# Kernel tuning notes

Measured on AMD Instinct MI355X. Metric: run time of the kernel, lower is better.

The kernel has to match this reference:

```python
import jax, jax.numpy as jnp
import numpy as np

IMG_W = 224
STRIDE = 16
NUM_HEADS = 12
# 196 grid centers, x-major order: [(x, y) for x in ... for y in ...]
_xs = np.arange(STRIDE // 2, IMG_W, STRIDE)
GRIDS = jnp.asarray(np.array([(x, y) for x in _xs for y in _xs], dtype=np.float32))  # [196, 2]


def setup_inputs() -> dict:
    key = jax.random.key(0)
    ks = jax.random.split(key, 8)
    B, N, C = 256, 198, 768
    s = 0.02
    return {
        "x": jax.random.normal(ks[0], (B, N, C), dtype=jnp.float32),
        "w_qkv": jax.random.normal(ks[1], (C, 3 * C), dtype=jnp.float32) * s,  # qkv_bias=False
        "w_proj": jax.random.normal(ks[2], (C, C), dtype=jnp.float32) * s,
        "b_proj": jax.random.normal(ks[3], (C,), dtype=jnp.float32) * s,
        "w_D": jax.random.normal(ks[4], (C, 3), dtype=jnp.float32) * s,
        "b_D": jax.random.normal(ks[5], (3,), dtype=jnp.float32) * s,
        "w_cen": jax.random.normal(ks[6], (C, 6), dtype=jnp.float32) * s,
        "b_cen": jax.random.normal(ks[7], (6,), dtype=jnp.float32) * s,
    }


def reference(x, w_qkv, w_proj, b_proj, w_D, b_D, w_cen, b_cen):
    B, N, C = x.shape
    H = NUM_HEADS
    dh = C // H
    scale = dh ** (-0.5)

    qkv = (x @ w_qkv).reshape(B, N, 3, H, dh).transpose(2, 0, 3, 1, 4)  # [3,B,H,N,dh]
    q, k, v = qkv[0], qkv[1], qkv[2]

    attn = jnp.einsum('bhnd,bhmd->bhnm', q, k) * scale
    attn = jax.nn.softmax(attn, axis=-1)  # [B,H,N,N]

    # CLS-token query, heads concatenated: q.permute(2,0,1,3).reshape(N,B,C)[0]
    q0 = q[:, :, 0, :].reshape(B, C)
    D = IMG_W * jax.nn.sigmoid(q0 @ w_D + b_D)                      # [B,3]
    cen = jax.nn.sigmoid((q0 @ w_cen + b_cen).reshape(B, 3, 2))     # [B,3,2]

    # mixture-of-gaussian blobs over 196 patch grid positions
    sigma = (D / 2.0)[..., None]                                    # [B,3,1]
    coord = cen * (IMG_W - 1)                                       # [B,3,2]
    dist = ((coord[:, :, None, :] - GRIDS[None, None]) ** 2).sum(-1)  # [B,3,196]
    mgb = jnp.exp(-dist / (2.0 * sigma ** 2)) / 2.0 / 3.14 / sigma ** 2
    mgb = mgb / mgb.sum(-1, keepdims=True)
    mgb = mgb.sum(axis=1) / 3.0                                     # [B,196]
    mgb = jnp.concatenate([jnp.ones((B, 2), mgb.dtype), mgb], axis=1)  # [B,N]

    # head-score reweighting of the CLS attention row
    hs = attn[:, :, 0, :].transpose(1, 0, 2)   # [H,B,N] == permute(1,2,0,3) squeezed
    hs = hs * mgb[None]                        # broadcast over heads
    hs = hs / hs.sum(-1, keepdims=True)
    # replicate torch masked_scatter flat-order semantics:
    # source flattened in (h,b,n) order is written into target positions in (b,h,n) order
    new_row = hs.reshape(-1).reshape(B, H, N)
    attn = attn.at[:, :, 0, :].set(new_row)

    out = jnp.einsum('bhnm,bhmd->bhnd', attn, v)      # [B,H,N,dh]
    out = out.transpose(0, 2, 1, 3).reshape(B, N, C)
    out = out @ w_proj + b_proj
    return cen, attn[:, :, 0, :], out
```

## Files before the change

### kernel.cpp

```cpp
#include <hip/hip_runtime.h>
#include <cstdint>
#include <cstddef>

typedef __attribute__((ext_vector_type(4))) float  f32x4;
typedef __attribute__((ext_vector_type(8))) __bf16 bf16x8;
typedef __attribute__((ext_vector_type(4))) __bf16 bf16x4;

#define MFMA16(A, B, C) __builtin_amdgcn_mfma_f32_16x16x32_bf16((A), (B), (C), 0, 0, 0)

#define GLOAD_LDS16(gp, lp)                                        \
    __builtin_amdgcn_global_load_lds(                              \
        (const __attribute__((address_space(1))) void*)(gp),       \
        (__attribute__((address_space(3))) void*)(lp), 16, 0, 0)

#define NB 256
#define NN 198
#define NC 768
#define NH 12

__global__ __launch_bounds__(256) void cast_to_bf16(const float* __restrict__ in,
                                                    __bf16* __restrict__ out, int n8) {
    int i = blockIdx.x * 256 + threadIdx.x;
    if (i < n8) {
        const float4 f0 = reinterpret_cast<const float4*>(in)[i * 2];
        const float4 f1 = reinterpret_cast<const float4*>(in)[i * 2 + 1];
        bf16x8 h;
        h[0] = (__bf16)f0.x; h[1] = (__bf16)f0.y; h[2] = (__bf16)f0.z; h[3] = (__bf16)f0.w;
        h[4] = (__bf16)f1.x; h[5] = (__bf16)f1.y; h[6] = (__bf16)f1.z; h[7] = (__bf16)f1.w;
        reinterpret_cast<bf16x8*>(out)[i] = h;
    }
}

__global__ __launch_bounds__(256) void transpose_to_bf16(
    const float* __restrict__ in, __bf16* __restrict__ out, int R, int Cc) {
    __shared__ __bf16 tile[32][33];
    const int ntc = Cc >> 5;
    const int tc = blockIdx.x % ntc, tr = blockIdx.x / ntc;
    const int c0 = tc * 32, r0 = tr * 32;
    const int lx = threadIdx.x & 31, ly = threadIdx.x >> 5;
#pragma unroll
    for (int j = 0; j < 4; ++j)
        tile[ly + j * 8][lx] = (__bf16)in[(size_t)(r0 + ly + j * 8) * Cc + c0 + lx];
    __syncthreads();
#pragma unroll
    for (int j = 0; j < 4; ++j)
        out[(size_t)(c0 + ly + j * 8) * R + r0 + lx] = tile[lx][ly + j * 8];
}

__global__ __launch_bounds__(512, 2) void gemm_qkv_v7(
    const __bf16* __restrict__ xb, const __bf16* __restrict__ wT,
    __bf16* __restrict__ qb, __bf16* __restrict__ kb, __bf16* __restrict__ vb,
    float* __restrict__ q0) {
    __shared__ __bf16 As[2][256 * 64];
    __shared__ __bf16 Bs[2][256 * 64];
    const int bid = blockIdx.x;
    const int xcd = bid & 7, lin = bid >> 3;
    const int wgid = (xcd < 6 ? xcd * 223 : 6 * 223 + (xcd - 6) * 222) + lin;
    const int brow = (wgid / 9) * 256;
    const int bcol = (wgid % 9) * 256;
    const int tid = threadIdx.x, lane = tid & 63, wid = tid >> 6;
    const int wr = wid >> 2, wc = wid & 3;
    const int lr = lane & 15, lg = lane >> 4;

    const int srow = tid >> 3;
    const int sslot = (tid & 7) ^ ((tid >> 3) & 7);
    const __bf16* aSrc = xb + (size_t)(brow + srow) * 768 + sslot * 8;
    const __bf16* bSrc = wT + (size_t)(bcol + srow) * 768 + sslot * 8;
    const int key = lr & 7;

    f32x4 acc[8][4] = {};

#define STAGE7(buf, kk0)                                                       \
    {                                                                          \
        __bf16* aD = &As[buf][wid * 512];                                      \
        __bf16* bD = &Bs[buf][wid * 512];                                      \
        _Pragma("unroll")                                                      \
        for (int j = 0; j < 4; ++j) {                                          \
            GLOAD_LDS16(aSrc + (size_t)j * 64 * 768 + (kk0), aD + j * 4096);   \
            GLOAD_LDS16(bSrc + (size_t)j * 64 * 768 + (kk0), bD + j * 4096);   \
        }                                                                      \
    }

#define LDA7(f0, f1, f2, f3, m0)                                               \
    f0 = *reinterpret_cast<const bf16x8*>(                                     \
        Ab + (wr * 128 + (m0) * 16 + lr) * 64 + ((lg ^ key) * 8));             \
    f1 = *reinterpret_cast<const bf16x8*>(                                     \
        Ab + (wr * 128 + (m0) * 16 + lr) * 64 + (((4 + lg) ^ key) * 8));       \
    f2 = *reinterpret_cast<const bf16x8*>(                                     \
        Ab + (wr * 128 + (m0) * 16 + 16 + lr) * 64 + ((lg ^ key) * 8));        \
    f3 = *reinterpret_cast<const bf16x8*>(                                     \
        Ab + (wr * 128 + (m0) * 16 + 16 + lr) * 64 + (((4 + lg) ^ key) * 8));

#define MFMA_PHASE7(f0, f1, f2, f3, m0)                                        \
    __builtin_amdgcn_s_setprio(1);                                             \
    _Pragma("unroll")                                                          \
    for (int nt = 0; nt < 4; ++nt) acc[(m0)][nt]     = MFMA16(f0, bfr[0][nt], acc[(m0)][nt]);     \
    _Pragma("unroll")                                                          \
    for (int nt = 0; nt < 4; ++nt) acc[(m0)][nt]     = MFMA16(f1, bfr[1][nt], acc[(m0)][nt]);     \
    _Pragma("unroll")                                                          \
    for (int nt = 0; nt < 4; ++nt) acc[(m0) + 1][nt] = MFMA16(f2, bfr[0][nt], acc[(m0) + 1][nt]); \
    _Pragma("unroll")                                                          \
    for (int nt = 0; nt < 4; ++nt) acc[(m0) + 1][nt] = MFMA16(f3, bfr[1][nt], acc[(m0) + 1][nt]); \
    __builtin_amdgcn_s_setprio(0);

    STAGE7(0, 0);
    STAGE7(1, 64);
    for (int tau = 0; tau < 12; ++tau) {
        const int b = tau & 1;
        if (tau == 11) asm volatile("s_waitcnt vmcnt(0)" ::: "memory");
        else           asm volatile("s_waitcnt vmcnt(8)" ::: "memory");
        __builtin_amdgcn_s_barrier();
        __builtin_amdgcn_sched_barrier(0);
        const __bf16* Ab = As[b];
        const __bf16* Bb = Bs[b];
        bf16x8 bfr[2][4];
#pragma unroll
        for (int kk = 0; kk < 2; ++kk)
#pragma unroll
            for (int nt = 0; nt < 4; ++nt)
                bfr[kk][nt] = *reinterpret_cast<const bf16x8*>(
                    Bb + (wc * 64 + nt * 16 + lr) * 64 + (((kk * 4 + lg) ^ key) * 8));
        bf16x8 a0, a1, a2, a3, b0, b1, b2, b3;
        LDA7(a0, a1, a2, a3, 0);
        LDA7(b0, b1, b2, b3, 2);
        asm volatile("s_waitcnt lgkmcnt(4)" ::: "memory");
        __builtin_amdgcn_sched_barrier(0);
        MFMA_PHASE7(a0, a1, a2, a3, 0);
        LDA7(a0, a1, a2, a3, 4);
        asm volatile("s_waitcnt lgkmcnt(4)" ::: "memory");
        __builtin_amdgcn_sched_barrier(0);
        MFMA_PHASE7(b0, b1, b2, b3, 2);
        LDA7(b0, b1, b2, b3, 6);
        asm volatile("s_waitcnt lgkmcnt(4)" ::: "memory");
        __builtin_amdgcn_sched_barrier(0);
        MFMA_PHASE7(a0, a1, a2, a3, 4);
        asm volatile("s_waitcnt lgkmcnt(0)" ::: "memory");
        __builtin_amdgcn_sched_barrier(0);
        __builtin_amdgcn_s_barrier();
        __builtin_amdgcn_sched_barrier(0);
        if (tau < 10) STAGE7(b, (tau + 2) * 64);
        MFMA_PHASE7(b0, b1, b2, b3, 6);
    }
#undef STAGE7

#pragma unroll
    for (int mt = 0; mt < 8; ++mt) {
        int grow0 = brow + wr * 128 + mt * 16 + lg * 4;
        int bbs[4], nns[4];
#pragma unroll
        for (int r = 0; r < 4; ++r) {
            bbs[r] = (grow0 + r) / 198;
            nns[r] = (grow0 + r) % 198;
        }
#pragma unroll
        for (int nt = 0; nt < 4; ++nt) {
            int gcol = bcol + wc * 64 + nt * 16 + lr;
            int sidx = gcol / 768;
            int rem  = gcol % 768;
            __bf16* dstbuf = (sidx == 0) ? qb : (sidx == 1) ? kb : vb;
            int hh = rem >> 6, dd = rem & 63;
#pragma unroll
            for (int r = 0; r < 4; ++r) {
                float val = acc[mt][nt][r];
                dstbuf[(((size_t)bbs[r] * 12 + hh) * 198 + nns[r]) * 64 + dd] = (__bf16)val;
                if (sidx == 0 && nns[r] == 0) q0[bbs[r] * 768 + rem] = val;
            }
        }
    }
}

__global__ __launch_bounds__(256) void mgb_kernel(
    const float* __restrict__ q0, const float* __restrict__ wD,
    const float* __restrict__ bD, const float* __restrict__ wcen,
    const float* __restrict__ bcen, float* __restrict__ cen_out,
    float* __restrict__ mgb) {
    const int b = blockIdx.x, t = threadIdx.x;
    __shared__ float qs[768];
    __shared__ float red[256];
    __shared__ float vals[9];
    qs[t]       = q0[b * 768 + t];
    qs[t + 256] = q0[b * 768 + t + 256];
    qs[t + 512] = q0[b * 768 + t + 512];
    __syncthreads();
    for (int j = 0; j < 9; ++j) {
        float p;
        if (j < 3)
            p = qs[t] * wD[t * 3 + j] + qs[t + 256] * wD[(t + 256) * 3 + j] +
                qs[t + 512] * wD[(t + 512) * 3 + j];
        else {
            int c = j - 3;
            p = qs[t] * wcen[t * 6 + c] + qs[t + 256] * wcen[(t + 256) * 6 + c] +
                qs[t + 512] * wcen[(t + 512) * 6 + c];
        }
        red[t] = p;
        __syncthreads();
        for (int off = 128; off > 0; off >>= 1) {
            if (t < off) red[t] += red[t + off];
            __syncthreads();
        }
        if (t == 0) {
            float bias = (j < 3) ? bD[j] : bcen[j - 3];
            vals[j] = 1.f / (1.f + __expf(-(red[0] + bias)));
        }
        __syncthreads();
    }
    if (t < 6) cen_out[b * 6 + t] = vals[3 + t];

    float e3[3] = {0.f, 0.f, 0.f};
    if (t < 196) {
        float gx = 8.f + 16.f * (float)(t / 14);
        float gy = 8.f + 16.f * (float)(t % 14);
#pragma unroll
        for (int j = 0; j < 3; ++j) {
            float sig = 112.f * vals[j];
            float cx = vals[3 + 2 * j] * 223.f;
            float cy = vals[3 + 2 * j + 1] * 223.f;
            float dx = cx - gx, dy = cy - gy;
            e3[j] = __expf(-(dx * dx + dy * dy) / (2.f * sig * sig));
        }
    }
    float js[3];
    for (int j = 0; j < 3; ++j) {
        red[t] = e3[j];
        __syncthreads();
        for (int off = 128; off > 0; off >>= 1) {
            if (t < off) red[t] += red[t + off];
            __syncthreads();
        }
        js[j] = red[0];
        __syncthreads();
    }
    if (t < 196) {
        float m = (e3[0] / js[0] + e3[1] / js[1] + e3[2] / js[2]) * (1.f / 3.f);
        mgb[(size_t)b * 198 + 2 + t] = m;
    }
    if (t < 2) mgb[(size_t)b * 198 + t] = 1.f;
}

__global__ __launch_bounds__(256) void attn_kernel(
    const __bf16* __restrict__ qb, const __bf16* __restrict__ kb,
    const __bf16* __restrict__ vb, float* __restrict__ p0,
    __bf16* __restrict__ outp) {
    __shared__ __bf16 Klds[208 * 64];
    __shared__ __bf16 Vt[64][216];
    __shared__ __bf16 Plds[4][16][216];
    const int bh = blockIdx.x;
    const int b = bh / 12, h = bh % 12;
    const __bf16* Qp = qb + (size_t)bh * NN * 64;
    const __bf16* Kp = kb + (size_t)bh * NN * 64;
    const __bf16* Vp = vb + (size_t)bh * NN * 64;
    const int tid = threadIdx.x, lane = tid & 63, wid = tid >> 6;
    const int lr = lane & 15, lg = lane >> 4;

    {
        const int rsub = wid * 8 + (lane >> 3);
        const int sl   = ((lane & 7) ^ ((lane >> 3) & 7)) * 8;
#pragma unroll
        for (int i = 0; i < 7; ++i) {
            if (i < 6 || wid < 2) {
                int row = i * 32 + rsub;
                int rowc = row < 198 ? row : 197;
                GLOAD_LDS16(Kp + (size_t)rowc * 64 + sl,
                            Klds + (size_t)i * 2048 + wid * 512);
            }
        }
    }

    for (int i = tid; i < 104 * 8; i += 256) {
        int key2 = (i >> 3) * 2, d0 = (i & 7) << 3;
        int kr0 = key2 < 198 ? key2 : 197;
        int kr1 = key2 + 1 < 198 ? key2 + 1 : 197;
        bf16x8 h0 = *reinterpret_cast<const bf16x8*>(Vp + kr0 * 64 + d0);
        bf16x8 h1 = *reinterpret_cast<const bf16x8*>(Vp + kr1 * 64 + d0);
#pragma unroll
        for (int j = 0; j < 8; ++j) {
            union { __bf16 hh[2]; unsigned u; } pk;
            pk.hh[0] = h0[j]; pk.hh[1] = h1[j];
            *reinterpret_cast<unsigned*>(&Vt[d0 + j][key2]) = pk.u;
        }
    }
    __syncthreads();

    for (int ch = wid; ch < 13; ch += 4) {
        int n0 = ch * 16;
        int qrow = n0 + lr; if (qrow > 197) qrow = 197;
        bf16x8 qf0 = *reinterpret_cast<const bf16x8*>(Qp + qrow * 64 + lg * 8);
        bf16x8 qf1 = *reinterpret_cast<const bf16x8*>(Qp + qrow * 64 + 32 + lg * 8);
        f32x4 sa[13];
#pragma unroll
        for (int t2 = 0; t2 < 13; ++t2) {
            int krow = t2 * 16 + lr;
            const int kx = lr & 7;
            bf16x8 kf0 = *reinterpret_cast<const bf16x8*>(
                Klds + krow * 64 + ((lg ^ kx) * 8));
            bf16x8 kf1 = *reinterpret_cast<const bf16x8*>(
                Klds + krow * 64 + (((4 + lg) ^ kx) * 8));
            f32x4 a = (f32x4){0.f, 0.f, 0.f, 0.f};
            a = MFMA16(kf0, qf0, a);
            a = MFMA16(kf1, qf1, a);
            sa[t2] = a;
        }
        float rmax = -1e30f;
#pragma unroll
        for (int t2 = 0; t2 < 13; ++t2)
#pragma unroll
            for (int r = 0; r < 4; ++r) {
                int key = t2 * 16 + lg * 4 + r;
                float vv = (key < 198) ? sa[t2][r] * 0.125f : -1e30f;
                sa[t2][r] = vv;
                rmax = fmaxf(rmax, vv);
            }
        rmax = fmaxf(rmax, __shfl_xor(rmax, 16));
        rmax = fmaxf(rmax, __shfl_xor(rmax, 32));
        float rsum = 0.f;
#pragma unroll
        for (int t2 = 0; t2 < 13; ++t2)
#pragma unroll
            for (int r = 0; r < 4; ++r) {
                float e = __expf(sa[t2][r] - rmax);
                sa[t2][r] = e;
                rsum += e;
            }
        rsum += __shfl_xor(rsum, 16);
        rsum += __shfl_xor(rsum, 32);
        float inv = 1.f / rsum;

        if (ch == 0 && lr == 0) {
#pragma unroll
            for (int t2 = 0; t2 < 13; ++t2)
#pragma unroll
                for (int r = 0; r < 4; ++r) {
                    int key = t2 * 16 + lg * 4 + r;
                    if (key < 198) p0[(size_t)bh * 198 + key] = sa[t2][r] * inv;
                }
        }
#pragma unroll
        for (int t2 = 0; t2 < 13; ++t2) {
            bf16x4 pk;
#pragma unroll
            for (int r = 0; r < 4; ++r) pk[r] = (__bf16)(sa[t2][r] * inv);
            *reinterpret_cast<bf16x4*>(&Plds[wid][lr][t2 * 16 + lg * 4]) = pk;
        }
        asm volatile("s_waitcnt lgkmcnt(0)" ::: "memory");

        f32x4 o[4];
#pragma unroll
        for (int mt = 0; mt < 4; ++mt) o[mt] = (f32x4){0.f, 0.f, 0.f, 0.f};
#pragma unroll
        for (int ks = 0; ks < 7; ++ks) {
            int kbase = ks * 32 + lg * 8;
            bf16x8 pf;
            if (kbase < 208)
                pf = *reinterpret_cast<const bf16x8*>(&Plds[wid][lr][kbase]);
            else {
#pragma unroll
                for (int j = 0; j < 8; ++j) pf[j] = (__bf16)0.f;
            }
#pragma unroll
            for (int mt = 0; mt < 4; ++mt) {
                bf16x8 vf;
                if (kbase < 208)
                    vf = *reinterpret_cast<const bf16x8*>(&Vt[mt * 16 + lr][kbase]);
                else {
#pragma unroll
                    for (int j = 0; j < 8; ++j) vf[j] = (__bf16)0.f;
                }
                o[mt] = MFMA16(vf, pf, o[mt]);
            }
        }
        int qg = n0 + lr;
        if (qg < 198) {
            __bf16* dst = outp + ((size_t)b * 198 + qg) * 768 + h * 64;
#pragma unroll
            for (int mt = 0; mt < 4; ++mt) {
                bf16x4 pk;
#pragma unroll
                for (int r = 0; r < 4; ++r) pk[r] = (__bf16)o[mt][r];
                *reinterpret_cast<bf16x4*>(dst + mt * 16 + lg * 4) = pk;
            }
        }
    }
}

__global__ __launch_bounds__(64) void reweight_kernel(
    const float* __restrict__ p0, const float* __restrict__ mgb,
    const __bf16* __restrict__ vb, float* __restrict__ attn_out,
    __bf16* __restrict__ outp) {
    const int t = blockIdx.x;
    const int b = t / 12, h = t % 12;
    const int h2 = t >> 8, b2 = t & 255;
    const int lane = threadIdx.x;
    __shared__ float nr[198];
    const float* pr = p0 + (size_t)(b2 * 12 + h2) * 198;
    const float* mr = mgb + (size_t)b2 * 198;
    float w[4];
    float ssum = 0.f;
#pragma unroll
    for (int i = 0; i < 4; ++i) {
        int n = lane + 64 * i;
        float xv = (n < 198) ? pr[n] * mr[n] : 0.f;
        w[i] = xv;
        ssum += xv;
    }
#pragma unroll
    for (int m = 1; m < 64; m <<= 1) ssum += __shfl_xor(ssum, m);
    float inv = 1.f / ssum;
#pragma unroll
    for (int i = 0; i < 4; ++i) {
        int n = lane + 64 * i;
        if (n < 198) {
            float xv = w[i] * inv;
            nr[n] = xv;
            attn_out[(size_t)t * 198 + n] = xv;
        }
    }
    __syncthreads();
    const __bf16* vp = vb + (size_t)t * 198 * 64;
    float acc = 0.f;
    for (int n = 0; n < 198; ++n) acc += nr[n] * (float)vp[n * 64 + lane];
    outp[((size_t)b * 198) * 768 + h * 64 + lane] = (__bf16)acc;
}

__global__ __launch_bounds__(256, 3) void gemm_proj_v8(
    const __bf16* __restrict__ A, const __bf16* __restrict__ wT,
    const float* __restrict__ bias, float* __restrict__ out) {
    __shared__ __bf16 As[2][128 * 32];
    __shared__ __bf16 Bs[2][128 * 32];
    const int bid = blockIdx.x;
    const int wg  = (bid & 7) * 297 + (bid >> 3);
    const int brow = (wg / 6) * 128;
    const int bcol = (wg % 6) * 128;
    const int tid = threadIdx.x, lane = tid & 63, wid = tid >> 6;
    const int wm = wid >> 1, wn = wid & 1;
    const int lr = lane & 15, lg = lane >> 4;

    const int srow = tid >> 2;
    const int sslot = (tid & 3) ^ ((tid >> 3) & 3);
    const __bf16* aSrc = A  + (size_t)(brow + srow) * 768 + sslot * 8;
    const __bf16* bSrc = wT + (size_t)(bcol + srow) * 768 + sslot * 8;
    const int rkey = (lr >> 1) & 3;

    f32x4 acc[4][4] = {};

#define STAGE_P6(buf, kk0)                                                    \
    {                                                                         \
        __bf16* aD = &As[buf][wid * 512];                                     \
        __bf16* bD = &Bs[buf][wid * 512];                                     \
        GLOAD_LDS16(aSrc + (kk0), aD);                                        \
        GLOAD_LDS16(bSrc + (kk0), bD);                                        \
        GLOAD_LDS16(aSrc + (size_t)64 * 768 + (kk0), aD + 2048);              \
        GLOAD_LDS16(bSrc + (size_t)64 * 768 + (kk0), bD + 2048);              \
    }

#define COMPUTE_P6(buf)                                                       \
    {                                                                         \
        const __bf16* Ab = As[buf];                                           \
        const __bf16* Bb = Bs[buf];                                           \
        bf16x8 af[4], bfv[4];                                                 \
        _Pragma("unroll")                                                     \
        for (int nt = 0; nt < 4; ++nt)                                        \
            bfv[nt] = *reinterpret_cast<const bf16x8*>(                       \
                Bb + (wn * 64 + nt * 16 + lr) * 32 + ((lg ^ rkey) * 8));      \
        _Pragma("unroll")                                                     \
        for (int mt = 0; mt < 4; ++mt)                                        \
            af[mt] = *reinterpret_cast<const bf16x8*>(                        \
                Ab + (wm * 64 + mt * 16 + lr) * 32 + ((lg ^ rkey) * 8));      \
        __builtin_amdgcn_s_setprio(1);                                        \
        _Pragma("unroll")                                                     \
        for (int mt = 0; mt < 4; ++mt)                                        \
            _Pragma("unroll")                                                 \
            for (int nt = 0; nt < 4; ++nt)                                    \
                acc[mt][nt] = MFMA16(af[mt], bfv[nt], acc[mt][nt]);           \
        __builtin_amdgcn_s_setprio(0);                                        \
    }

    STAGE_P6(0, 0);
    STAGE_P6(1, 32);
    for (int tau = 0; tau < 24; ++tau) {
        if (tau == 23) asm volatile("s_waitcnt vmcnt(0)" ::: "memory");
        else           asm volatile("s_waitcnt vmcnt(4)" ::: "memory");
        __builtin_amdgcn_s_barrier();
        __builtin_amdgcn_sched_barrier(0);
        COMPUTE_P6(tau & 1);
        __builtin_amdgcn_sched_barrier(0);
        __builtin_amdgcn_s_barrier();
        __builtin_amdgcn_sched_barrier(0);
        if (tau < 22) STAGE_P6(tau & 1, (tau + 2) * 32);
    }
#undef STAGE_P6
#undef COMPUTE_P6

#pragma unroll
    for (int mt = 0; mt < 4; ++mt) {
#pragma unroll
        for (int nt = 0; nt < 4; ++nt) {
            int gcol = bcol + wn * 64 + nt * 16 + lr;
            float bv = bias[gcol];
#pragma unroll
            for (int r = 0; r < 4; ++r) {
                int grow = brow + wm * 64 + mt * 16 + lg * 4 + r;
                out[(size_t)grow * 768 + gcol] = acc[mt][nt][r] + bv;
            }
        }
    }
}

extern "C" void kernel_launch(void* const* d_in, const int* in_sizes, int n_in,
                              void* d_out, int out_size, void* d_ws, size_t ws_size,
                              hipStream_t stream) {
    const float* x      = (const float*)d_in[0];
    const float* w_qkv  = (const float*)d_in[1];
    const float* w_proj = (const float*)d_in[2];
    const float* b_proj = (const float*)d_in[3];
    const float* w_D    = (const float*)d_in[4];
    const float* b_D    = (const float*)d_in[5];
    const float* w_cen  = (const float*)d_in[6];
    const float* b_cen  = (const float*)d_in[7];

    float* out      = (float*)d_out;
    float* cen_out  = out;
    float* attn_out = out + 1536;
    float* proj_out = out + 1536 + 608256;

    char* ws = (char*)d_ws;
    size_t off = 0;
    auto carve = [&](size_t bytes) {
        void* p = ws + off;
        off += (bytes + 255) & ~(size_t)255;
        return p;
    };
    __bf16* wqkvT  = (__bf16*)carve((size_t)2304 * 768 * 2);
    __bf16* wprojT = (__bf16*)carve((size_t)768 * 768 * 2);
    __bf16* qb     = (__bf16*)carve((size_t)3072 * 198 * 64 * 2);
    __bf16* kb     = (__bf16*)carve((size_t)3072 * 198 * 64 * 2);
    __bf16* vb     = (__bf16*)carve((size_t)3072 * 198 * 64 * 2);
    __bf16* outp   = (__bf16*)carve((size_t)50688 * 768 * 2);
    float*  q0     = (float*)carve((size_t)256 * 768 * 4);
    float*  mgb    = (float*)carve((size_t)256 * 198 * 4);
    float*  p0     = (float*)carve((size_t)3072 * 198 * 4);

    __bf16* xb = outp;

    cast_to_bf16<<<(50688 * 768 / 8 + 255) / 256, 256, 0, stream>>>(x, xb, 50688 * 768 / 8);
    transpose_to_bf16<<<(2304 / 32) * (768 / 32), 256, 0, stream>>>(w_qkv, wqkvT, 768, 2304);
    transpose_to_bf16<<<(768 / 32) * (768 / 32), 256, 0, stream>>>(w_proj, wprojT, 768, 768);
    gemm_qkv_v7<<<1782, 512, 0, stream>>>(xb, wqkvT, qb, kb, vb, q0);
    mgb_kernel<<<256, 256, 0, stream>>>(q0, w_D, b_D, w_cen, b_cen, cen_out, mgb);
    attn_kernel<<<3072, 256, 0, stream>>>(qb, kb, vb, p0, outp);
    reweight_kernel<<<3072, 64, 0, stream>>>(p0, mgb, vb, attn_out, outp);
    gemm_proj_v8<<<2376, 256, 0, stream>>>(outp, wprojT, b_proj, proj_out);
}
```

Measured before the change: 517.9 us.

## Load QKV GEMM B operand directly from global into registers, dropping its LDS staging

The weight (B) tile of the QKV GEMM is no longer staged through LDS. Each wave now reads its B fragments straight from global memory into registers every k-step, which halves LDS use and removes the B-side async copies. The waits and barriers are restructured around this. In exchange, every wave issues redundant global loads for the same weight rows, and a full vmcnt(0) wait each iteration may expose global latency.

```diff
diff --git a/kernel.cpp b/kernel.cpp
--- a/kernel.cpp
+++ b/kernel.cpp
@@ -47,12 +47,11 @@
         out[(size_t)(c0 + ly + j * 8) * R + r0 + lx] = tile[lx][ly + j * 8];
 }
 
-__global__ __launch_bounds__(512, 2) void gemm_qkv_v7(
+__global__ __launch_bounds__(512, 2) void gemm_qkv_v10(
     const __bf16* __restrict__ xb, const __bf16* __restrict__ wT,
     __bf16* __restrict__ qb, __bf16* __restrict__ kb, __bf16* __restrict__ vb,
     float* __restrict__ q0) {
     __shared__ __bf16 As[2][256 * 64];
-    __shared__ __bf16 Bs[2][256 * 64];
     const int bid = blockIdx.x;
     const int xcd = bid & 7, lin = bid >> 3;
     const int wgid = (xcd < 6 ? xcd * 223 : 6 * 223 + (xcd - 6) * 222) + lin;
@@ -65,20 +64,17 @@
     const int srow = tid >> 3;
     const int sslot = (tid & 7) ^ ((tid >> 3) & 7);
     const __bf16* aSrc = xb + (size_t)(brow + srow) * 768 + sslot * 8;
-    const __bf16* bSrc = wT + (size_t)(bcol + srow) * 768 + sslot * 8;
+    const __bf16* wB   = wT + (size_t)(bcol + wc * 64 + lr) * 768 + lg * 8;
     const int key = lr & 7;
 
     f32x4 acc[8][4] = {};
 
-#define STAGE7(buf, kk0)                                                       \
+#define STAGEA(buf, kk0)                                                       \
     {                                                                          \
         __bf16* aD = &As[buf][wid * 512];                                      \
-        __bf16* bD = &Bs[buf][wid * 512];                                      \
         _Pragma("unroll")                                                      \
-        for (int j = 0; j < 4; ++j) {                                          \
+        for (int j = 0; j < 4; ++j)                                            \
             GLOAD_LDS16(aSrc + (size_t)j * 64 * 768 + (kk0), aD + j * 4096);   \
-            GLOAD_LDS16(bSrc + (size_t)j * 64 * 768 + (kk0), bD + j * 4096);   \
-        }                                                                      \
     }
 
 #define LDA7(f0, f1, f2, f3, m0)                                               \
@@ -103,26 +99,28 @@
     for (int nt = 0; nt < 4; ++nt) acc[(m0) + 1][nt] = MFMA16(f3, bfr[1][nt], acc[(m0) + 1][nt]); \
     __builtin_amdgcn_s_setprio(0);
 
-    STAGE7(0, 0);
-    STAGE7(1, 64);
+    STAGEA(0, 0);
+    STAGEA(1, 64);
+    asm volatile("s_waitcnt vmcnt(4)" ::: "memory");
+    __builtin_amdgcn_s_barrier();
+    __builtin_amdgcn_sched_barrier(0);
+
     for (int tau = 0; tau < 12; ++tau) {
         const int b = tau & 1;
-        if (tau == 11) asm volatile("s_waitcnt vmcnt(0)" ::: "memory");
-        else           asm volatile("s_waitcnt vmcnt(8)" ::: "memory");
-        __builtin_amdgcn_s_barrier();
-        __builtin_amdgcn_sched_barrier(0);
         const __bf16* Ab = As[b];
-        const __bf16* Bb = Bs[b];
+        const int k0 = tau * 64;
         bf16x8 bfr[2][4];
 #pragma unroll
         for (int kk = 0; kk < 2; ++kk)
 #pragma unroll
             for (int nt = 0; nt < 4; ++nt)
                 bfr[kk][nt] = *reinterpret_cast<const bf16x8*>(
-                    Bb + (wc * 64 + nt * 16 + lr) * 64 + (((kk * 4 + lg) ^ key) * 8));
+                    wB + (size_t)(nt * 16) * 768 + k0 + kk * 32);
         bf16x8 a0, a1, a2, a3, b0, b1, b2, b3;
         LDA7(a0, a1, a2, a3, 0);
         LDA7(b0, b1, b2, b3, 2);
+        asm volatile("s_waitcnt vmcnt(0)" ::: "memory");
+        __builtin_amdgcn_sched_barrier(0);
         asm volatile("s_waitcnt lgkmcnt(4)" ::: "memory");
         __builtin_amdgcn_sched_barrier(0);
         MFMA_PHASE7(a0, a1, a2, a3, 0);
@@ -138,10 +136,10 @@
         __builtin_amdgcn_sched_barrier(0);
         __builtin_amdgcn_s_barrier();
         __builtin_amdgcn_sched_barrier(0);
-        if (tau < 10) STAGE7(b, (tau + 2) * 64);
+        if (tau < 10) STAGEA(b, (tau + 2) * 64);
         MFMA_PHASE7(b0, b1, b2, b3, 6);
     }
-#undef STAGE7
+#undef STAGEA
 
 #pragma unroll
     for (int mt = 0; mt < 8; ++mt) {
@@ -544,7 +542,7 @@
     cast_to_bf16<<<(50688 * 768 / 8 + 255) / 256, 256, 0, stream>>>(x, xb, 50688 * 768 / 8);
     transpose_to_bf16<<<(2304 / 32) * (768 / 32), 256, 0, stream>>>(w_qkv, wqkvT, 768, 2304);
     transpose_to_bf16<<<(768 / 32) * (768 / 32), 256, 0, stream>>>(w_proj, wprojT, 768, 768);
-    gemm_qkv_v7<<<1782, 512, 0, stream>>>(xb, wqkvT, qb, kb, vb, q0);
+    gemm_qkv_v10<<<1782, 512, 0, stream>>>(xb, wqkvT, qb, kb, vb, q0);
     mgb_kernel<<<256, 256, 0, stream>>>(q0, w_D, b_D, w_cen, b_cen, cen_out, mgb);
     attn_kernel<<<3072, 256, 0, stream>>>(qb, kb, vb, p0, outp);
     reweight_kernel<<<3072, 64, 0, stream>>>(p0, mgb, vb, attn_out, outp);
```

New measurement: 598.8 us. 15.6% more time.
